# Kernel tuning notes

Hardware: AMD Instinct MI355X
Metric: run time of the kernel (lower is better)

Reference implementation:

```python
import jax, jax.numpy as jnp
from jax import lax
import numpy as np

B, T, IN, H, C, L = 128, 256, 256, 512, 10, 2


def _xavier(key, shape):
    fan_out, fan_in = shape
    bound = float(np.sqrt(6.0 / (fan_in + fan_out)))
    return jax.random.uniform(key, shape, jnp.float32, -bound, bound)


def setup_inputs() -> dict:
    key = jax.random.key(0)
    ks = jax.random.split(key, 8)
    x = jax.random.normal(ks[0], (B, T, IN), jnp.float32)
    # PyTorch LSTM params: W_ih [4H, in], W_hh [4H, H], biases zero-init per module
    W_ih0 = _xavier(ks[1], (4 * H, IN))
    W_hh0 = _xavier(ks[2], (4 * H, H))
    b_ih0 = jnp.zeros((4 * H,), jnp.float32)
    b_hh0 = jnp.zeros((4 * H,), jnp.float32)
    W_ih1 = _xavier(ks[3], (4 * H, H))
    W_hh1 = _xavier(ks[4], (4 * H, H))
    b_ih1 = jnp.zeros((4 * H,), jnp.float32)
    b_hh1 = jnp.zeros((4 * H,), jnp.float32)
    W_fc = _xavier(ks[5], (C, H))
    b_fc = jnp.zeros((C,), jnp.float32)
    return {
        "x": x,
        "W_ih0": W_ih0, "W_hh0": W_hh0, "b_ih0": b_ih0, "b_hh0": b_hh0,
        "W_ih1": W_ih1, "W_hh1": W_hh1, "b_ih1": b_ih1, "b_hh1": b_hh1,
        "W_fc": W_fc, "b_fc": b_fc,
    }


def _lstm_layer(x, W_ih, W_hh, b_ih, b_hh):
    # x: [B, T, D_in] -> hidden sequence [B, T, H]
    Bq = x.shape[0]
    Hh = W_hh.shape[1]
    # precompute input contributions for all timesteps (one big GEMM)
    xg = jnp.einsum('btd,gd->btg', x, W_ih) + b_ih + b_hh  # [B, T, 4H]
    xg = jnp.swapaxes(xg, 0, 1)  # [T, B, 4H]

    def step(carry, xg_t):
        h, c = carry
        gates = xg_t + h @ W_hh.T  # [B, 4H]
        i, f, g, o = jnp.split(gates, 4, axis=-1)  # PyTorch gate order: i,f,g,o
        i = jax.nn.sigmoid(i)
        f = jax.nn.sigmoid(f)
        g = jnp.tanh(g)
        o = jax.nn.sigmoid(o)
        c = f * c + i * g
        h = o * jnp.tanh(c)
        return (h, c), h

    h0 = jnp.zeros((Bq, Hh), x.dtype)
    c0 = jnp.zeros((Bq, Hh), x.dtype)
    _, hs = lax.scan(step, (h0, c0), xg)  # hs: [T, B, H]
    return jnp.swapaxes(hs, 0, 1)


def reference(x, W_ih0, W_hh0, b_ih0, b_hh0, W_ih1, W_hh1, b_ih1, b_hh1, W_fc, b_fc):
    h = _lstm_layer(x, W_ih0, W_hh0, b_ih0, b_hh0)
    h = _lstm_layer(h, W_ih1, W_hh1, b_ih1, b_hh1)
    last = h[:, -1, :]  # [B, H]
    logits = last @ W_fc.T + b_fc  # [B, C]
    return jax.nn.log_softmax(logits, axis=1)
```

## Files before the change

kernel.cpp:

```cpp
#include <hip/hip_runtime.h>

#define B_ 128
#define T_ 256
#define IN_ 256
#define H_ 512
#define G4_ 2048
#define TC_ 16
#define NCHUNK_ 16

typedef __attribute__((ext_vector_type(8))) short short8v;
typedef __attribute__((ext_vector_type(4))) float float4v;
typedef unsigned short ushort_t;

static constexpr size_t OFF_XG0 = 0;
static constexpr size_t OFF_XG1 = OFF_XG0 + (size_t)B_ * TC_ * G4_ / 2;
static constexpr size_t OFF_H0C = OFF_XG1 + (size_t)B_ * TC_ * G4_ / 2;
static constexpr size_t OFF_HB0 = OFF_H0C + (size_t)B_ * TC_ * H_ / 2;
static constexpr size_t OFF_HB1 = OFF_HB0 + (size_t)B_ * H_;
static constexpr size_t OFF_C0  = OFF_HB1 + (size_t)B_ * H_;
static constexpr size_t OFF_C1  = OFF_C0 + (size_t)B_ * H_;
static constexpr size_t OFF_WF0 = OFF_C1 + (size_t)B_ * H_;
static constexpr size_t OFF_WF1 = OFF_WF0 + (size_t)G4_ * H_ / 2;
static constexpr size_t OFF_WI0 = OFF_WF1 + (size_t)G4_ * H_ / 2;
static constexpr size_t OFF_WI1 = OFF_WI0 + (size_t)G4_ * IN_ / 2;
static constexpr size_t OFF_END = OFF_WI1 + (size_t)G4_ * H_ / 2;

__device__ __forceinline__ unsigned int bfr(float f) {
  unsigned int u = __float_as_uint(f);
  return (u + 0x7fffu + ((u >> 16) & 1u)) >> 16;
}
__device__ __forceinline__ float bf2f(unsigned int u) {
  return __uint_as_float(u << 16);
}

__global__ __launch_bounds__(256) void pack_whh3(
    const float* __restrict__ W, uint4* __restrict__ WF) {
  const int idx = blockIdx.x * 256 + threadIdx.x;
  const int l  = idx & 63;
  const int ks = (idx >> 6) & 15;
  const int g  = (idx >> 10) & 3;
  const int ct = idx >> 12;
  const int row = g * H_ + ct * 16 + (l & 15);
  const int k0  = ks * 32 + (l >> 4) * 8;
  const float* s = W + (size_t)row * H_ + k0;
  uint4 o;
  o.x = bfr(s[0]) | (bfr(s[1]) << 16);
  o.y = bfr(s[2]) | (bfr(s[3]) << 16);
  o.z = bfr(s[4]) | (bfr(s[5]) << 16);
  o.w = bfr(s[6]) | (bfr(s[7]) << 16);
  WF[idx] = o;
}

__global__ __launch_bounds__(256) void pack_wih(
    const float* __restrict__ W, uint4* __restrict__ WF, int K) {
  const int idx = blockIdx.x * 256 + threadIdx.x;
  const int ksn = K >> 5;
  const int l  = idx & 63;
  const int ks = (idx >> 6) & (ksn - 1);
  const int nt = idx >> 6 >> (K == 512 ? 4 : 3);
  const int row = nt * 16 + (l & 15);
  const int k0  = ks * 32 + (l >> 4) * 8;
  const float* s = W + (size_t)row * K + k0;
  uint4 o;
  o.x = bfr(s[0]) | (bfr(s[1]) << 16);
  o.y = bfr(s[2]) | (bfr(s[3]) << 16);
  o.z = bfr(s[4]) | (bfr(s[5]) << 16);
  o.w = bfr(s[6]) | (bfr(s[7]) << 16);
  WF[idx] = o;
}

__device__ __forceinline__ void gemm_dev(
    uint4* Ash, const void* Av, int abf, int K, int T_A, int t0,
    const short8v* WF, const float* b1, const float* b2,
    ushort_t* Cw, int gbid, int tid) {
  const int xcd = gbid & 7;
  const int q   = gbid >> 3;
  const int n0  = (xcd * 4 + (q & 3)) * 64;
  const int m0  = (q >> 2) * 64;
  const int ksn = K >> 5;
  const int npass = K >> 8;

  const int lane = tid & 63;
  const int w = tid >> 6;
  const int ar = lane & 15;
  const int koct = lane >> 4;
  const int nt = (n0 >> 4) + w;
  const short8v* wf = WF + (size_t)nt * ksn * 64 + lane;
  float4v acc0 = {0,0,0,0}, acc1 = {0,0,0,0}, acc2 = {0,0,0,0}, acc3 = {0,0,0,0};

  for (int p = 0; p < npass; ++p) {
    if (p) __syncthreads();
    for (int idx = tid; idx < 2048; idx += 256) {
      const int r = idx >> 5, c = idx & 31;
      const int m = m0 + r;
      const size_t arow = (size_t)(m >> 4) * T_A + t0 + (m & 15);
      const size_t koff = (size_t)p * 256 + c * 8;
      uint4 val;
      if (abf) {
        val = *(const uint4*)((const ushort_t*)Av + arow * K + koff);
      } else {
        const float* ap = (const float*)Av + arow * K + koff;
        const float4 lo = *(const float4*)ap;
        const float4 hi = *(const float4*)(ap + 4);
        val.x = bfr(lo.x) | (bfr(lo.y) << 16);
        val.y = bfr(lo.z) | (bfr(lo.w) << 16);
        val.z = bfr(hi.x) | (bfr(hi.y) << 16);
        val.w = bfr(hi.z) | (bfr(hi.w) << 16);
      }
      Ash[(r << 5) + (c ^ (r & 7))] = val;
    }
    __syncthreads();
#pragma unroll 4
    for (int ksl = 0; ksl < 8; ++ksl) {
      const short8v bv = wf[(size_t)(p * 8 + ksl) * 64];
      const int cc = ksl * 4 + koct;
      const short8v a0 = *(const short8v*)&Ash[((ar +  0) << 5) + (cc ^ ((ar +  0) & 7))];
      const short8v a1 = *(const short8v*)&Ash[((ar + 16) << 5) + (cc ^ ((ar + 16) & 7))];
      const short8v a2 = *(const short8v*)&Ash[((ar + 32) << 5) + (cc ^ ((ar + 32) & 7))];
      const short8v a3 = *(const short8v*)&Ash[((ar + 48) << 5) + (cc ^ ((ar + 48) & 7))];
      acc0 = __builtin_amdgcn_mfma_f32_16x16x32_bf16(a0, bv, acc0, 0, 0, 0);
      acc1 = __builtin_amdgcn_mfma_f32_16x16x32_bf16(a1, bv, acc1, 0, 0, 0);
      acc2 = __builtin_amdgcn_mfma_f32_16x16x32_bf16(a2, bv, acc2, 0, 0, 0);
      acc3 = __builtin_amdgcn_mfma_f32_16x16x32_bf16(a3, bv, acc3, 0, 0, 0);
    }
  }
  const int dcol = lane & 15, drow = (lane >> 4) * 4;
  const int n = n0 + w * 16 + dcol;
  const float bs = b1[n] + b2[n];
#pragma unroll
  for (int rr = 0; rr < 4; ++rr) {
    const float v[4] = {acc0[rr], acc1[rr], acc2[rr], acc3[rr]};
#pragma unroll
    for (int mb = 0; mb < 4; ++mb)
      Cw[(size_t)(m0 + mb * 16 + drow + rr) * G4_ + n] = (ushort_t)bfr(v[mb] + bs);
  }
}

__global__ __launch_bounds__(256) void gemm_dual(
    const float* __restrict__ x, const short8v* __restrict__ WI0,
    const float* __restrict__ bi0, const float* __restrict__ bh0,
    ushort_t* __restrict__ xg0w, int t0,
    const ushort_t* __restrict__ h0c, const short8v* __restrict__ WI1,
    const float* __restrict__ bi1, const float* __restrict__ bh1,
    ushort_t* __restrict__ xg1w, int do1) {
  __shared__ uint4 Ash[2048];
  int bid = blockIdx.x;
  if (do1) {
    if (bid < 1024) {
      gemm_dev(Ash, h0c, 1, H_, TC_, 0, WI1, bi1, bh1, xg1w, bid, threadIdx.x);
      return;
    }
    bid -= 1024;
  }
  gemm_dev(Ash, x, 0, IN_, T_, t0, WI0, bi0, bh0, xg0w, bid, threadIdx.x);
}

__global__ __launch_bounds__(256) void lstm_step2(
    const short8v* __restrict__ WF0, const ushort_t* __restrict__ xg0,
    const ushort_t* __restrict__ h0p, ushort_t* __restrict__ h0n,
    float* __restrict__ cs0, ushort_t* __restrict__ h0c,
    const short8v* __restrict__ WF1, const ushort_t* __restrict__ xg1,
    const ushort_t* __restrict__ h1p, ushort_t* __restrict__ h1n,
    float* __restrict__ cs1, int tl, int mode) {
  __shared__ ushort_t hsh[16 * 512];
  __shared__ float gl[4][16][17];
  const int bid = blockIdx.x;
  const int layer = (mode == 0) ? (bid >> 8) : (mode - 1);
  const int xcd = bid & 7;
  const int ctl = (bid >> 3) & 3;
  const int bt  = (bid >> 5) & 7;
  const int ct  = xcd * 4 + ctl;
  const int b0  = bt * 16;

  const short8v* WF; const ushort_t* xg; const ushort_t* hprev;
  ushort_t* hnext; float* cst;
  if (layer == 0) { WF = WF0; xg = xg0; hprev = h0p; hnext = h0n; cst = cs0; }
  else            { WF = WF1; xg = xg1; hprev = h1p; hnext = h1n; cst = cs1; }

  const int tid = threadIdx.x;
  const int tb = tid >> 4, thc = tid & 15;
  const int bb = b0 + tb;
  const int hcol = ct * 16 + thc;
  const ushort_t* xr = xg + ((size_t)bb * TC_ + tl) * G4_ + hcol;
  const float xi  = bf2f(xr[0]);
  const float xf  = bf2f(xr[512]);
  const float xgv = bf2f(xr[1024]);
  const float xo  = bf2f(xr[1536]);
  const float cin = cst[(size_t)bb * H_ + hcol];

  const uint4* hp4 = (const uint4*)hprev + (size_t)b0 * 64;
#pragma unroll
  for (int j = 0; j < 4; ++j) {
    const int idx = tid + j * 256;
    const int r = idx >> 6, c = idx & 63;
    *(uint4*)&hsh[(r * 64 + (c ^ (r & 7))) * 8] = hp4[(size_t)r * 64 + c];
  }
  __syncthreads();

  const int lane = tid & 63;
  const int g = tid >> 6;
  const int ar = lane & 15;
  const int koct = lane >> 4;
  float4v acc = {0.f, 0.f, 0.f, 0.f};
  const short8v* wf = WF + ((size_t)(ct * 4 + g) * 16) * 64 + lane;
#pragma unroll
  for (int ks = 0; ks < 16; ++ks) {
    const int c16 = ks * 4 + koct;
    const short8v av = *(const short8v*)&hsh[(ar * 64 + (c16 ^ (ar & 7))) * 8];
    const short8v bv = wf[(size_t)ks * 64];
    acc = __builtin_amdgcn_mfma_f32_16x16x32_bf16(av, bv, acc, 0, 0, 0);
  }
  const int drow = (lane >> 4) * 4, dcol = lane & 15;
#pragma unroll
  for (int rr = 0; rr < 4; ++rr) gl[g][drow + rr][dcol] = acc[rr];
  __syncthreads();

  {
    const float gi = gl[0][tb][thc] + xi;
    const float gf = gl[1][tb][thc] + xf;
    const float gg = gl[2][tb][thc] + xgv;
    const float go = gl[3][tb][thc] + xo;
    const float iv = 1.f / (1.f + __expf(-gi));
    const float fv = 1.f / (1.f + __expf(-gf));
    const float gv = tanhf(gg);
    const float ov = 1.f / (1.f + __expf(-go));
    const float cn = fv * cin + iv * gv;
    const float hv = ov * tanhf(cn);
    cst[(size_t)bb * H_ + hcol] = cn;
    const ushort_t hb = (ushort_t)bfr(hv);
    hnext[(size_t)bb * H_ + hcol] = hb;
    if (layer == 0) h0c[((size_t)bb * TC_ + tl) * H_ + hcol] = hb;
  }
}

__global__ __launch_bounds__(64) void fc_logsoftmax(
    const ushort_t* __restrict__ h, const float* __restrict__ Wfc,
    const float* __restrict__ bfc, float* __restrict__ out) {
  const int b = blockIdx.x, lane = threadIdx.x;
  const uint4 hv = *(const uint4*)(h + (size_t)b * H_ + lane * 8);
  const float hf[8] = {
      bf2f(hv.x & 0xffffu), bf2f(hv.x >> 16), bf2f(hv.y & 0xffffu), bf2f(hv.y >> 16),
      bf2f(hv.z & 0xffffu), bf2f(hv.z >> 16), bf2f(hv.w & 0xffffu), bf2f(hv.w >> 16)};
  float logits[10];
#pragma unroll
  for (int cc = 0; cc < 10; ++cc) {
    const float* wr = Wfc + (size_t)cc * H_ + lane * 8;
    const float4 w0 = *(const float4*)wr;
    const float4 w1 = *(const float4*)(wr + 4);
    float v = hf[0] * w0.x + hf[1] * w0.y + hf[2] * w0.z + hf[3] * w0.w +
              hf[4] * w1.x + hf[5] * w1.y + hf[6] * w1.z + hf[7] * w1.w;
#pragma unroll
    for (int off = 32; off; off >>= 1) v += __shfl_xor(v, off);
    logits[cc] = v + bfc[cc];
  }
  float m = logits[0];
#pragma unroll
  for (int cc = 1; cc < 10; ++cc) m = fmaxf(m, logits[cc]);
  float s = 0.f;
#pragma unroll
  for (int cc = 0; cc < 10; ++cc) s += __expf(logits[cc] - m);
  const float lse = m + __logf(s);
  if (lane < 10) out[(size_t)b * 10 + lane] = logits[lane] - lse;
}

extern "C" void kernel_launch(void* const* d_in, const int* in_sizes, int n_in,
                              void* d_out, int out_size, void* d_ws, size_t ws_size,
                              hipStream_t stream) {
  const float* x    = (const float*)d_in[0];
  const float* Wih0 = (const float*)d_in[1];
  const float* Whh0 = (const float*)d_in[2];
  const float* bih0 = (const float*)d_in[3];
  const float* bhh0 = (const float*)d_in[4];
  const float* Wih1 = (const float*)d_in[5];
  const float* Whh1 = (const float*)d_in[6];
  const float* bih1 = (const float*)d_in[7];
  const float* bhh1 = (const float*)d_in[8];
  const float* Wfc  = (const float*)d_in[9];
  const float* bfc  = (const float*)d_in[10];

  float* ws = (float*)d_ws;
  ushort_t* XG0 = (ushort_t*)(ws + OFF_XG0);
  ushort_t* XG1 = (ushort_t*)(ws + OFF_XG1);
  ushort_t* h0c = (ushort_t*)(ws + OFF_H0C);
  ushort_t* hb0 = (ushort_t*)(ws + OFF_HB0);
  ushort_t* hb1 = (ushort_t*)(ws + OFF_HB1);
  float* c0 = ws + OFF_C0;
  float* c1 = ws + OFF_C1;
  short8v* wf0 = (short8v*)(ws + OFF_WF0);
  short8v* wf1 = (short8v*)(ws + OFF_WF1);
  short8v* wi0 = (short8v*)(ws + OFF_WI0);
  short8v* wi1 = (short8v*)(ws + OFF_WI1);

  hipMemsetAsync(hb0, 0, (OFF_WF0 - OFF_HB0) * sizeof(float), stream);
  pack_whh3<<<512, 256, 0, stream>>>(Whh0, (uint4*)wf0);
  pack_whh3<<<512, 256, 0, stream>>>(Whh1, (uint4*)wf1);
  pack_wih<<<256, 256, 0, stream>>>(Wih0, (uint4*)wi0, IN_);
  pack_wih<<<512, 256, 0, stream>>>(Wih1, (uint4*)wi1, H_);

  const size_t BHu = (size_t)B_ * H_;
  for (int ch = 0; ch < NCHUNK_; ++ch) {
    const int t0 = ch * TC_;
    const int do1 = (ch > 0) ? 1 : 0;
    gemm_dual<<<do1 ? 2048 : 1024, 256, 0, stream>>>(
        x, wi0, bih0, bhh0, XG0, t0,
        h0c, wi1, bih1, bhh1, XG1, do1);
    for (int t = 0; t < TC_; ++t) {
      const int sg0 = t0 + t + 1;
      const int sg1 = sg0 - TC_;
      const int mode = (ch == 0) ? 1 : 0;
      const int nblk = (ch == 0) ? 256 : 512;
      lstm_step2<<<nblk, 256, 0, stream>>>(
          wf0, XG0, hb0 + ((sg0 - 1) & 1) * BHu, hb0 + (sg0 & 1) * BHu, c0, h0c,
          wf1, XG1, hb1 + ((sg1 - 1) & 1) * BHu, hb1 + (sg1 & 1) * BHu, c1,
          t, mode);
    }
  }
  gemm_dual<<<1024, 256, 0, stream>>>(
      x, wi0, bih0, bhh0, XG0, -1,
      h0c, wi1, bih1, bhh1, XG1, 1);
  for (int t = 0; t < TC_; ++t) {
    const int sg1 = (NCHUNK_ - 1) * TC_ + t + 1;
    lstm_step2<<<256, 256, 0, stream>>>(
        wf0, XG0, hb0, hb0, c0, h0c,
        wf1, XG1, hb1 + ((sg1 - 1) & 1) * BHu, hb1 + (sg1 & 1) * BHu, c1,
        t, 2);
  }
  fc_logsoftmax<<<dim3(B_), 64, 0, stream>>>(hb1, Wfc, bfc, (float*)d_out);
}
```

Baseline: 1.376 ms.

## Interleave gate outputs in xg layout and widen LSTM step blocks to 32 columns

The input-projection GEMM now writes its output with the four gates interleaved per hidden column, so each step thread fetches its four gate preactivations in one 8-byte load instead of four scattered loads. The recurrent step kernel now uses 512-thread blocks covering 32 hidden columns, which halves the block count and loads the shared h tile half as many times per output. The trade-off is fewer blocks per step, which lowers parallelism across CUs, and more scattered 2-byte stores in the GEMM epilogue.

```diff
diff --git a/kernel.cpp b/kernel.cpp
--- a/kernel.cpp
+++ b/kernel.cpp
@@ -126,13 +126,15 @@
   }
   const int dcol = lane & 15, drow = (lane >> 4) * 4;
   const int n = n0 + w * 16 + dcol;
+  const int gate = n >> 9, hc = n & 511;
   const float bs = b1[n] + b2[n];
 #pragma unroll
   for (int rr = 0; rr < 4; ++rr) {
     const float v[4] = {acc0[rr], acc1[rr], acc2[rr], acc3[rr]};
 #pragma unroll
     for (int mb = 0; mb < 4; ++mb)
-      Cw[(size_t)(m0 + mb * 16 + drow + rr) * G4_ + n] = (ushort_t)bfr(v[mb] + bs);
+      Cw[((size_t)(m0 + mb * 16 + drow + rr) * 512 + hc) * 4 + gate] =
+          (ushort_t)bfr(v[mb] + bs);
   }
 }
 
@@ -155,7 +157,7 @@
   gemm_dev(Ash, x, 0, IN_, T_, t0, WI0, bi0, bh0, xg0w, bid, threadIdx.x);
 }
 
-__global__ __launch_bounds__(256) void lstm_step2(
+__global__ __launch_bounds__(512) void lstm_step2(
     const short8v* __restrict__ WF0, const ushort_t* __restrict__ xg0,
     const ushort_t* __restrict__ h0p, ushort_t* __restrict__ h0n,
     float* __restrict__ cs0, ushort_t* __restrict__ h0c,
@@ -163,14 +165,15 @@
     const ushort_t* __restrict__ h1p, ushort_t* __restrict__ h1n,
     float* __restrict__ cs1, int tl, int mode) {
   __shared__ ushort_t hsh[16 * 512];
-  __shared__ float gl[4][16][17];
+  __shared__ float gl[2][4][16][17];
   const int bid = blockIdx.x;
-  const int layer = (mode == 0) ? (bid >> 8) : (mode - 1);
-  const int xcd = bid & 7;
-  const int ctl = (bid >> 3) & 3;
-  const int bt  = (bid >> 5) & 7;
-  const int ct  = xcd * 4 + ctl;
-  const int b0  = bt * 16;
+  int lbid = bid, layer;
+  if (mode == 0) { layer = bid >> 7; lbid = bid & 127; } else layer = mode - 1;
+  const int xcd  = lbid & 7;
+  const int q    = lbid >> 3;
+  const int ct32 = xcd * 2 + (q & 1);
+  const int bt   = q >> 1;
+  const int b0   = bt * 16;
 
   const short8v* WF; const ushort_t* xg; const ushort_t* hprev;
   ushort_t* hnext; float* cst;
@@ -178,31 +181,33 @@
   else            { WF = WF1; xg = xg1; hprev = h1p; hnext = h1n; cst = cs1; }
 
   const int tid = threadIdx.x;
-  const int tb = tid >> 4, thc = tid & 15;
+  const int tb = tid >> 5, thc = tid & 31;
   const int bb = b0 + tb;
-  const int hcol = ct * 16 + thc;
-  const ushort_t* xr = xg + ((size_t)bb * TC_ + tl) * G4_ + hcol;
-  const float xi  = bf2f(xr[0]);
-  const float xf  = bf2f(xr[512]);
-  const float xgv = bf2f(xr[1024]);
-  const float xo  = bf2f(xr[1536]);
+  const int hcol = ct32 * 32 + thc;
+  const uint2 xq = *(const uint2*)(xg + (((size_t)bb * TC_ + tl) * 512 + hcol) * 4);
+  const float xi  = bf2f(xq.x & 0xffffu);
+  const float xf  = bf2f(xq.x >> 16);
+  const float xgv = bf2f(xq.y & 0xffffu);
+  const float xo  = bf2f(xq.y >> 16);
   const float cin = cst[(size_t)bb * H_ + hcol];
 
   const uint4* hp4 = (const uint4*)hprev + (size_t)b0 * 64;
 #pragma unroll
-  for (int j = 0; j < 4; ++j) {
-    const int idx = tid + j * 256;
+  for (int j = 0; j < 2; ++j) {
+    const int idx = tid + j * 512;
     const int r = idx >> 6, c = idx & 63;
     *(uint4*)&hsh[(r * 64 + (c ^ (r & 7))) * 8] = hp4[(size_t)r * 64 + c];
   }
   __syncthreads();
 
   const int lane = tid & 63;
-  const int g = tid >> 6;
+  const int w  = tid >> 6;
+  const int cs = w >> 2;
+  const int g  = w & 3;
   const int ar = lane & 15;
   const int koct = lane >> 4;
   float4v acc = {0.f, 0.f, 0.f, 0.f};
-  const short8v* wf = WF + ((size_t)(ct * 4 + g) * 16) * 64 + lane;
+  const short8v* wf = WF + ((size_t)((ct32 * 2 + cs) * 4 + g) * 16) * 64 + lane;
 #pragma unroll
   for (int ks = 0; ks < 16; ++ks) {
     const int c16 = ks * 4 + koct;
@@ -212,14 +217,15 @@
   }
   const int drow = (lane >> 4) * 4, dcol = lane & 15;
 #pragma unroll
-  for (int rr = 0; rr < 4; ++rr) gl[g][drow + rr][dcol] = acc[rr];
+  for (int rr = 0; rr < 4; ++rr) gl[cs][g][drow + rr][dcol] = acc[rr];
   __syncthreads();
 
   {
-    const float gi = gl[0][tb][thc] + xi;
-    const float gf = gl[1][tb][thc] + xf;
-    const float gg = gl[2][tb][thc] + xgv;
-    const float go = gl[3][tb][thc] + xo;
+    const int cs_t = thc >> 4, t16 = thc & 15;
+    const float gi = gl[cs_t][0][tb][t16] + xi;
+    const float gf = gl[cs_t][1][tb][t16] + xf;
+    const float gg = gl[cs_t][2][tb][t16] + xgv;
+    const float go = gl[cs_t][3][tb][t16] + xo;
     const float iv = 1.f / (1.f + __expf(-gi));
     const float fv = 1.f / (1.f + __expf(-gf));
     const float gv = tanhf(gg);
@@ -308,8 +314,8 @@
       const int sg0 = t0 + t + 1;
       const int sg1 = sg0 - TC_;
       const int mode = (ch == 0) ? 1 : 0;
-      const int nblk = (ch == 0) ? 256 : 512;
-      lstm_step2<<<nblk, 256, 0, stream>>>(
+      const int nblk = (ch == 0) ? 128 : 256;
+      lstm_step2<<<nblk, 512, 0, stream>>>(
           wf0, XG0, hb0 + ((sg0 - 1) & 1) * BHu, hb0 + (sg0 & 1) * BHu, c0, h0c,
           wf1, XG1, hb1 + ((sg1 - 1) & 1) * BHu, hb1 + (sg1 & 1) * BHu, c1,
           t, mode);
@@ -320,7 +326,7 @@
       h0c, wi1, bih1, bhh1, XG1, 1);
   for (int t = 0; t < TC_; ++t) {
     const int sg1 = (NCHUNK_ - 1) * TC_ + t + 1;
-    lstm_step2<<<256, 256, 0, stream>>>(
+    lstm_step2<<<128, 512, 0, stream>>>(
         wf0, XG0, hb0, hb0, c0, h0c,
         wf1, XG1, hb1 + ((sg1 - 1) & 1) * BHu, hb1 + (sg1 & 1) * BHu, c1,
         t, 2);
```

Result: slower. 1.582 ms (+15.0%).
